# Optimization experiments

Measured on AMD Instinct MI355X. Metric: run time of the kernel, lower is better.

Reference implementation:

```python
import jax, jax.numpy as jnp
import numpy as np

NODE = 100000
REL = 2000
E = 600000  # n_edges == triple_size
D = 128
DEPTH = 2
HEADS = 1


def setup_inputs() -> dict:
    key = jax.random.key(0)
    ks = jax.random.split(key, 8)
    features = jax.random.normal(ks[0], (NODE, D), jnp.float32)
    rel_emb = jax.random.normal(ks[1], (REL, D), jnp.float32)
    sp_val = jax.random.uniform(ks[2], (E,), jnp.float32)
    attn_kernels = jax.random.normal(ks[3], (DEPTH, HEADS, 3 * D), jnp.float32) * 0.1
    adj_src = jnp.sort(jax.random.randint(ks[4], (E,), 0, NODE))  # tf.segment_sum needs sorted ids
    adj_dst = jax.random.randint(ks[5], (E,), 0, NODE)
    sp_rel = jax.random.randint(ks[6], (E,), 0, REL)
    sp_row = jnp.arange(E)  # sparse (triple, rel) matrix row indices
    return dict(features=features, rel_emb=rel_emb, sp_val=sp_val,
                attn_kernels=attn_kernels, adj_src=adj_src, adj_dst=adj_dst,
                sp_rel=sp_rel, sp_row=sp_row)


def _segment_softmax(logits, seg, num):
    m = jax.ops.segment_max(logits, seg, num_segments=num)
    e = jnp.exp(logits - m[seg])
    s = jax.ops.segment_sum(e, seg, num_segments=num)
    return e / s[seg]


def reference(features, rel_emb, sp_val, attn_kernels, adj_src, adj_dst, sp_rel, sp_row):
    act = jax.nn.relu
    feats = act(features)
    outputs = [feats]
    for l in range(DEPTH):
        heads = []
        for h in range(HEADS):
            ak = attn_kernels[l, h]  # [3D]
            # sparse (triple x rel) @ rel_emb -> per-edge relation embedding [E, D]
            rels = jax.ops.segment_sum(sp_val[:, None] * rel_emb[sp_rel], sp_row,
                                       num_segments=E)
            # tf.nn.l2_normalize with eps 1e-12
            rels = rels * jax.lax.rsqrt(jnp.maximum(jnp.sum(rels * rels, axis=1,
                                                            keepdims=True), 1e-12))
            neighs = feats[adj_dst]  # [E, D]
            selfs = feats[adj_src]   # [E, D]
            # Householder-style reflection of neighbor features across rels
            proj = jnp.sum(neighs * rels, axis=1, keepdims=True) * rels
            neighs = neighs - 2.0 * proj
            # attention logits: concat([selfs, neighs, rels]) @ ak
            att = selfs @ ak[:D] + neighs @ ak[D:2 * D] + rels @ ak[2 * D:]
            a = _segment_softmax(att, adj_src, NODE)  # tf.sparse_softmax per row
            heads.append(jax.ops.segment_sum(neighs * a[:, None], adj_src,
                                             num_segments=NODE))
        feats = heads[0] if HEADS == 1 else jnp.concatenate(heads, axis=1)
        feats = act(feats)
        outputs.append(feats)
    return jnp.concatenate(outputs, axis=1)  # [NODE, D*(DEPTH+1)]
```

## Files before the change

### kernel.cpp

```cpp
#include <hip/hip_runtime.h>
#include <math.h>
#include <stdint.h>

#define NNODE 100000
#define NREL 2000
#define NEDGE 600000
#define DIM 128
#define OUTC 384

#define RELU_BLOCKS 12500
#define PRE_BLOCKS 500
#define ROW_BLOCKS ((NNODE + 1 + 255) / 256)

typedef float f32x2 __attribute__((ext_vector_type(2)));

__device__ __forceinline__ float wave_sum(float v) {
#pragma unroll
    for (int off = 32; off > 0; off >>= 1)
        v += __shfl_xor(v, off, 64);
    return v;
}

__device__ __forceinline__ unsigned short f2bf(float f) {
    unsigned b = __float_as_uint(f);
    return (unsigned short)((b + 0x7fffu + ((b >> 16) & 1u)) >> 16);
}
__device__ __forceinline__ unsigned pack2(float f0, float f1) {
    return (unsigned)f2bf(f0) | ((unsigned)f2bf(f1) << 16);
}
__device__ __forceinline__ f32x2 bf2(unsigned u) {
    f32x2 r;
    r.x = __uint_as_float(u << 16);
    r.y = __uint_as_float(u & 0xffff0000u);
    return r;
}

__global__ void k_setup(const float* __restrict__ f, const float* __restrict__ rel,
                        const float* __restrict__ attn, const int* __restrict__ adj_src,
                        float* __restrict__ out, unsigned short* __restrict__ fm,
                        unsigned short* __restrict__ relm,
                        float* __restrict__ relnorm2, float* __restrict__ rdB,
                        float* __restrict__ rdC,
                        float* __restrict__ selfdot0, float* __restrict__ neighdot0,
                        int* __restrict__ row_ptr) {
    int b = blockIdx.x;
    if (b < RELU_BLOCKS) {
        int idx = b * 256 + threadIdx.x;
        int n = idx >> 5;
        int q = idx & 31;
        float4 v = reinterpret_cast<const float4*>(f + (size_t)n * DIM)[q];
        v.x = fmaxf(v.x, 0.f); v.y = fmaxf(v.y, 0.f);
        v.z = fmaxf(v.z, 0.f); v.w = fmaxf(v.w, 0.f);
        reinterpret_cast<float4*>(out + (size_t)n * OUTC)[q] = v;
        uint2 p;
        p.x = pack2(v.x, v.y);
        p.y = pack2(v.z, v.w);
        reinterpret_cast<uint2*>(fm + (size_t)n * DIM)[q] = p;
        float4 a = reinterpret_cast<const float4*>(attn)[q];
        float4 bb = reinterpret_cast<const float4*>(attn + DIM)[q];
        float pa = v.x * a.x + v.y * a.y + v.z * a.z + v.w * a.w;
        float pb = v.x * bb.x + v.y * bb.y + v.z * bb.z + v.w * bb.w;
#pragma unroll
        for (int off = 1; off <= 16; off <<= 1) {
            pa += __shfl_xor(pa, off, 64);
            pb += __shfl_xor(pb, off, 64);
        }
        if (q == 0) { selfdot0[n] = pa; neighdot0[n] = pb; }
    } else if (b < RELU_BLOCKS + PRE_BLOCKS) {
        int wid = (b - RELU_BLOCKS) * 4 + (threadIdx.x >> 6);
        int lane = threadIdx.x & 63;
        float2 v = reinterpret_cast<const float2*>(rel + (size_t)wid * DIM)[lane];
        reinterpret_cast<unsigned*>(relm + (size_t)wid * DIM)[lane] = pack2(v.x, v.y);
        float2 b0 = reinterpret_cast<const float2*>(attn + DIM)[lane];
        float2 c0 = reinterpret_cast<const float2*>(attn + 2 * DIM)[lane];
        float2 b1 = reinterpret_cast<const float2*>(attn + 3 * DIM + DIM)[lane];
        float2 c1 = reinterpret_cast<const float2*>(attn + 3 * DIM + 2 * DIM)[lane];
        float n2  = wave_sum(v.x * v.x + v.y * v.y);
        float pb0 = wave_sum(v.x * b0.x + v.y * b0.y);
        float pc0 = wave_sum(v.x * c0.x + v.y * c0.y);
        float pb1 = wave_sum(v.x * b1.x + v.y * b1.y);
        float pc1 = wave_sum(v.x * c1.x + v.y * c1.y);
        if (lane == 0) {
            relnorm2[wid] = n2;
            rdB[wid] = pb0;        rdC[wid] = pc0;
            rdB[NREL + wid] = pb1; rdC[NREL + wid] = pc1;
        }
    } else {
        int n = (b - RELU_BLOCKS - PRE_BLOCKS) * 256 + threadIdx.x;
        if (n <= NNODE) {
            int lo = 0, hi = NEDGE;
            while (lo < hi) {
                int mid = (lo + hi) >> 1;
                if (adj_src[mid] < n) lo = mid + 1; else hi = mid;
            }
            row_ptr[n] = lo;
        }
    }
}

__global__ void k_edges(const float* __restrict__ sp_val, const int* __restrict__ sp_rel,
                        const int* __restrict__ adj_dst,
                        const float* __restrict__ relnorm2,
                        const float* __restrict__ rdB, const float* __restrict__ rdC,
                        float4* __restrict__ ed0, float4* __restrict__ ed1) {
    int e = blockIdx.x * blockDim.x + threadIdx.x;
    if (e >= NEDGE) return;
    float v = sp_val[e];
    int r = sp_rel[e];
    float n2 = relnorm2[r];
    float sc = v * rsqrtf(fmaxf(v * v * n2, 1e-12f));
    float q2 = 2.f * sc * sc;
    unsigned pk = ((unsigned)adj_dst[e] << 11) | (unsigned)r;
    float pkf = __uint_as_float(pk);
    ed0[e] = make_float4(sc * rdC[r],        q2 * rdB[r],        q2, pkf);
    ed1[e] = make_float4(sc * rdC[NREL + r], q2 * rdB[NREL + r], q2, pkf);
}

template<int USE_ED, int WRITE_NEXT>
__global__ void k_gat(const unsigned short* __restrict__ fin_m,
                      float* __restrict__ fout,
                      unsigned short* __restrict__ fout_m,
                      const unsigned short* __restrict__ relm,
                      const float4* __restrict__ edata,
                      const int* __restrict__ adj_dst, const int* __restrict__ sp_rel,
                      const float* __restrict__ sp_val, const float* __restrict__ relnorm2,
                      const float* __restrict__ rdB, const float* __restrict__ rdC,
                      const float* __restrict__ selfdot, const float* __restrict__ neighdot,
                      const int* __restrict__ row_ptr,
                      float* __restrict__ sd_n, float* __restrict__ nd_n,
                      const float* __restrict__ ak_next) {
    int wv = (blockIdx.x * blockDim.x + threadIdx.x) >> 6;
    int lane = threadIdx.x & 63;
    int g = lane >> 4, gl = lane & 15;
    int node = wv * 4 + g;
    if (node >= NNODE) return;
    int e0 = row_ptr[node], e1 = row_ptr[node + 1];
    float sd = selfdot[node];

    f32x2 acc0 = 0.f, acc1 = 0.f, acc2 = 0.f, acc3 = 0.f;
    float m = -3.0e38f, s = 0.f;

    uint4 fb = make_uint4(0, 0, 0, 0), rb = make_uint4(0, 0, 0, 0);
    float ab = 0.f, qb = 0.f, q2 = 0.f;
    int e = e0;
    if (e < e1) {
        int dst, r;
        if (USE_ED) {
            float4 ed = edata[e];
            unsigned pk = __float_as_uint(ed.w);
            dst = (int)(pk >> 11); r = (int)(pk & 2047u);
            ab = sd + ed.x + neighdot[dst];
            qb = ed.y; q2 = ed.z;
        } else {
            dst = adj_dst[e]; r = sp_rel[e];
            float v = sp_val[e];
            float sc = v * rsqrtf(fmaxf(v * v * relnorm2[r], 1e-12f));
            q2 = 2.f * sc * sc;
            qb = q2 * rdB[r];
            ab = sd + sc * rdC[r] + neighdot[dst];
        }
        fb = *reinterpret_cast<const uint4*>(fin_m + (size_t)dst * DIM + gl * 8);
        rb = *reinterpret_cast<const uint4*>(relm + (size_t)r * DIM + gl * 8);
    }
    while (e < e1) {
        int en = e + 1;
        bool more = en < e1;
        uint4 fb2 = make_uint4(0, 0, 0, 0), rb2 = make_uint4(0, 0, 0, 0);
        float ab2 = 0.f, qb2 = 0.f, q22 = 0.f;
        if (more) {
            int dst, r;
            if (USE_ED) {
                float4 ed = edata[en];
                unsigned pk = __float_as_uint(ed.w);
                dst = (int)(pk >> 11); r = (int)(pk & 2047u);
                ab2 = sd + ed.x + neighdot[dst];
                qb2 = ed.y; q22 = ed.z;
            } else {
                dst = adj_dst[en]; r = sp_rel[en];
                float v = sp_val[en];
                float sc = v * rsqrtf(fmaxf(v * v * relnorm2[r], 1e-12f));
                q22 = 2.f * sc * sc;
                qb2 = q22 * rdB[r];
                ab2 = sd + sc * rdC[r] + neighdot[dst];
            }
            fb2 = *reinterpret_cast<const uint4*>(fin_m + (size_t)dst * DIM + gl * 8);
            rb2 = *reinterpret_cast<const uint4*>(relm + (size_t)r * DIM + gl * 8);
        }
        f32x2 f0 = bf2(fb.x), f1 = bf2(fb.y), f2 = bf2(fb.z), f3 = bf2(fb.w);
        f32x2 r0 = bf2(rb.x), r1 = bf2(rb.y), r2 = bf2(rb.z), r3 = bf2(rb.w);
        f32x2 d2 = f0 * r0;
        d2 += f1 * r1;
        d2 += f2 * r2;
        d2 += f3 * r3;
        float dot = d2.x + d2.y;
        dot += __shfl_xor(dot, 1, 64);
        dot += __shfl_xor(dot, 2, 64);
        dot += __shfl_xor(dot, 4, 64);
        dot += __shfl_xor(dot, 8, 64);
        float att = ab - dot * qb;
        float k2 = dot * q2;
        float nm = fmaxf(m, att);
        float corr = __expf(m - nm);
        float w = __expf(att - nm);
        s = s * corr + w;
        acc0 = acc0 * corr + w * (f0 - k2 * r0);
        acc1 = acc1 * corr + w * (f1 - k2 * r1);
        acc2 = acc2 * corr + w * (f2 - k2 * r2);
        acc3 = acc3 * corr + w * (f3 - k2 * r3);
        m = nm;
        e = en;
        fb = fb2; rb = rb2; ab = ab2; qb = qb2; q2 = q22;
    }

    float inv = (s > 0.f) ? 1.f / s : 0.f;
    float o[8];
    o[0] = fmaxf(acc0.x * inv, 0.f); o[1] = fmaxf(acc0.y * inv, 0.f);
    o[2] = fmaxf(acc1.x * inv, 0.f); o[3] = fmaxf(acc1.y * inv, 0.f);
    o[4] = fmaxf(acc2.x * inv, 0.f); o[5] = fmaxf(acc2.y * inv, 0.f);
    o[6] = fmaxf(acc3.x * inv, 0.f); o[7] = fmaxf(acc3.y * inv, 0.f);
    float4* op = reinterpret_cast<float4*>(fout + (size_t)node * OUTC + gl * 8);
    op[0] = make_float4(o[0], o[1], o[2], o[3]);
    op[1] = make_float4(o[4], o[5], o[6], o[7]);
    if (WRITE_NEXT) {
        uint4 mw;
        mw.x = pack2(o[0], o[1]); mw.y = pack2(o[2], o[3]);
        mw.z = pack2(o[4], o[5]); mw.w = pack2(o[6], o[7]);
        *reinterpret_cast<uint4*>(fout_m + (size_t)node * DIM + gl * 8) = mw;
        const float4* aA = reinterpret_cast<const float4*>(ak_next) + gl * 2;
        const float4* aB = reinterpret_cast<const float4*>(ak_next + DIM) + gl * 2;
        float4 a0 = aA[0], a1 = aA[1], b0 = aB[0], b1 = aB[1];
        float pa = o[0] * a0.x + o[1] * a0.y + o[2] * a0.z + o[3] * a0.w
                 + o[4] * a1.x + o[5] * a1.y + o[6] * a1.z + o[7] * a1.w;
        float pb = o[0] * b0.x + o[1] * b0.y + o[2] * b0.z + o[3] * b0.w
                 + o[4] * b1.x + o[5] * b1.y + o[6] * b1.z + o[7] * b1.w;
#pragma unroll
        for (int off = 1; off <= 8; off <<= 1) {
            pa += __shfl_xor(pa, off, 64);
            pb += __shfl_xor(pb, off, 64);
        }
        if (gl == 0) { sd_n[node] = pa; nd_n[node] = pb; }
    }
}

extern "C" void kernel_launch(void* const* d_in, const int* in_sizes, int n_in,
                              void* d_out, int out_size, void* d_ws, size_t ws_size,
                              hipStream_t stream) {
    const float* features = (const float*)d_in[0];
    const float* rel_emb  = (const float*)d_in[1];
    const float* sp_val   = (const float*)d_in[2];
    const float* attn     = (const float*)d_in[3];
    const int*   adj_src  = (const int*)d_in[4];
    const int*   adj_dst  = (const int*)d_in[5];
    const int*   sp_rel   = (const int*)d_in[6];
    float* out = (float*)d_out;

    char* p = (char*)d_ws;
    unsigned short* mir0 = (unsigned short*)p; p += (size_t)NNODE * DIM * 2;
    unsigned short* mir1 = (unsigned short*)p; p += (size_t)NNODE * DIM * 2;
    unsigned short* relm = (unsigned short*)p; p += (size_t)NREL * DIM * 2;
    float* sd0      = (float*)p; p += (size_t)NNODE * 4;
    float* nd0      = (float*)p; p += (size_t)NNODE * 4;
    float* sd1      = (float*)p; p += (size_t)NNODE * 4;
    float* nd1      = (float*)p; p += (size_t)NNODE * 4;
    float* relnorm2 = (float*)p; p += (size_t)NREL * 4;
    float* rdB      = (float*)p; p += (size_t)2 * NREL * 4;
    float* rdC      = (float*)p; p += (size_t)2 * NREL * 4;
    int*   row_ptr  = (int*)p;   p += (size_t)(NNODE + 1) * 4;
    p = (char*)(((uintptr_t)p + 15) & ~(uintptr_t)15);
    float4* ed0 = (float4*)p; p += (size_t)NEDGE * 16;
    float4* ed1 = (float4*)p; p += (size_t)NEDGE * 16;
    size_t needed = (size_t)(p - (char*)d_ws);
    bool use_ed = (ws_size >= needed);

    k_setup<<<RELU_BLOCKS + PRE_BLOCKS + ROW_BLOCKS, 256, 0, stream>>>(
        features, rel_emb, attn, adj_src, out, mir0, relm,
        relnorm2, rdB, rdC, sd0, nd0, row_ptr);

    int gat_blocks = (NNODE / 4 * 64) / 256;

    if (use_ed) {
        k_edges<<<(NEDGE + 255) / 256, 256, 0, stream>>>(
            sp_val, sp_rel, adj_dst, relnorm2, rdB, rdC, ed0, ed1);
        k_gat<1, 1><<<gat_blocks, 256, 0, stream>>>(
            mir0, out + DIM, mir1, relm, ed0, adj_dst, sp_rel, sp_val, relnorm2,
            rdB, rdC, sd0, nd0, row_ptr, sd1, nd1, attn + 3 * DIM);
        k_gat<1, 0><<<gat_blocks, 256, 0, stream>>>(
            mir1, out + 2 * DIM, (unsigned short*)nullptr, relm, ed1, adj_dst, sp_rel,
            sp_val, relnorm2, rdB + NREL, rdC + NREL, sd1, nd1, row_ptr,
            (float*)nullptr, (float*)nullptr, (const float*)nullptr);
    } else {
        k_gat<0, 1><<<gat_blocks, 256, 0, stream>>>(
            mir0, out + DIM, mir1, relm, (const float4*)nullptr, adj_dst, sp_rel,
            sp_val, relnorm2, rdB, rdC, sd0, nd0, row_ptr, sd1, nd1, attn + 3 * DIM);
        k_gat<0, 0><<<gat_blocks, 256, 0, stream>>>(
            mir1, out + 2 * DIM, (unsigned short*)nullptr, relm, (const float4*)nullptr,
            adj_dst, sp_rel, sp_val, relnorm2, rdB + NREL, rdC + NREL, sd1, nd1, row_ptr,
            (float*)nullptr, (float*)nullptr, (const float*)nullptr);
    }
}
```

Measured before the change: 144.3 us.

## Drop self-term and running max from segment softmax, fold neighbor dot into edge data

The self-attention term is constant within each source-node segment, so it cancels in the softmax and is removed, along with the selfdot arrays. The online-softmax running max and rescaling are dropped, and exp2 is used with log2e pre-folded into the edge coefficients. The layer-0 neighbor dot is folded into the precomputed edge record, removing a gather per edge. Without max subtraction, large logits could overflow exp, and 32-bit index arithmetic replaces size_t.

After: 144.8 us. Within noise of the previous version (+0.3%).

```diff
diff --git a/kernel.cpp b/kernel.cpp
--- a/kernel.cpp
+++ b/kernel.cpp
@@ -7,6 +7,7 @@
 #define NEDGE 600000
 #define DIM 128
 #define OUTC 384
+#define LOG2E 1.4426950408889634f
 
 #define RELU_BLOCKS 12500
 #define PRE_BLOCKS 500
@@ -41,8 +42,7 @@
                         unsigned short* __restrict__ relm,
                         float* __restrict__ relnorm2, float* __restrict__ rdB,
                         float* __restrict__ rdC,
-                        float* __restrict__ selfdot0, float* __restrict__ neighdot0,
-                        int* __restrict__ row_ptr) {
+                        float* __restrict__ nd0, int* __restrict__ row_ptr) {
     int b = blockIdx.x;
     if (b < RELU_BLOCKS) {
         int idx = b * 256 + threadIdx.x;
@@ -56,16 +56,12 @@
         p.x = pack2(v.x, v.y);
         p.y = pack2(v.z, v.w);
         reinterpret_cast<uint2*>(fm + (size_t)n * DIM)[q] = p;
-        float4 a = reinterpret_cast<const float4*>(attn)[q];
         float4 bb = reinterpret_cast<const float4*>(attn + DIM)[q];
-        float pa = v.x * a.x + v.y * a.y + v.z * a.z + v.w * a.w;
         float pb = v.x * bb.x + v.y * bb.y + v.z * bb.z + v.w * bb.w;
 #pragma unroll
-        for (int off = 1; off <= 16; off <<= 1) {
-            pa += __shfl_xor(pa, off, 64);
+        for (int off = 1; off <= 16; off <<= 1)
             pb += __shfl_xor(pb, off, 64);
-        }
-        if (q == 0) { selfdot0[n] = pa; neighdot0[n] = pb; }
+        if (q == 0) nd0[n] = pb * LOG2E;
     } else if (b < RELU_BLOCKS + PRE_BLOCKS) {
         int wid = (b - RELU_BLOCKS) * 4 + (threadIdx.x >> 6);
         int lane = threadIdx.x & 63;
@@ -102,21 +98,24 @@
                         const int* __restrict__ adj_dst,
                         const float* __restrict__ relnorm2,
                         const float* __restrict__ rdB, const float* __restrict__ rdC,
+                        const float* __restrict__ nd0,
                         float4* __restrict__ ed0, float4* __restrict__ ed1) {
     int e = blockIdx.x * blockDim.x + threadIdx.x;
     if (e >= NEDGE) return;
     float v = sp_val[e];
     int r = sp_rel[e];
+    int dst = adj_dst[e];
     float n2 = relnorm2[r];
     float sc = v * rsqrtf(fmaxf(v * v * n2, 1e-12f));
     float q2 = 2.f * sc * sc;
-    unsigned pk = ((unsigned)adj_dst[e] << 11) | (unsigned)r;
+    float scl = sc * LOG2E, q2l = q2 * LOG2E;
+    unsigned pk = ((unsigned)dst << 11) | (unsigned)r;
     float pkf = __uint_as_float(pk);
-    ed0[e] = make_float4(sc * rdC[r],        q2 * rdB[r],        q2, pkf);
-    ed1[e] = make_float4(sc * rdC[NREL + r], q2 * rdB[NREL + r], q2, pkf);
-}
-
-template<int USE_ED, int WRITE_NEXT>
+    ed0[e] = make_float4(nd0[dst] + scl * rdC[r], q2l * rdB[r], q2, pkf);
+    ed1[e] = make_float4(scl * rdC[NREL + r], q2l * rdB[NREL + r], q2, pkf);
+}
+
+template<int USE_ED, int NDFOLD, int WRITE_NEXT>
 __global__ void k_gat(const unsigned short* __restrict__ fin_m,
                       float* __restrict__ fout,
                       unsigned short* __restrict__ fout_m,
@@ -125,20 +124,19 @@
                       const int* __restrict__ adj_dst, const int* __restrict__ sp_rel,
                       const float* __restrict__ sp_val, const float* __restrict__ relnorm2,
                       const float* __restrict__ rdB, const float* __restrict__ rdC,
-                      const float* __restrict__ selfdot, const float* __restrict__ neighdot,
+                      const float* __restrict__ ndpre,
                       const int* __restrict__ row_ptr,
-                      float* __restrict__ sd_n, float* __restrict__ nd_n,
-                      const float* __restrict__ ak_next) {
+                      float* __restrict__ nd_n,
+                      const float* __restrict__ akB_next) {
     int wv = (blockIdx.x * blockDim.x + threadIdx.x) >> 6;
     int lane = threadIdx.x & 63;
     int g = lane >> 4, gl = lane & 15;
     int node = wv * 4 + g;
     if (node >= NNODE) return;
     int e0 = row_ptr[node], e1 = row_ptr[node + 1];
-    float sd = selfdot[node];
 
     f32x2 acc0 = 0.f, acc1 = 0.f, acc2 = 0.f, acc3 = 0.f;
-    float m = -3.0e38f, s = 0.f;
+    float s = 0.f;
 
     uint4 fb = make_uint4(0, 0, 0, 0), rb = make_uint4(0, 0, 0, 0);
     float ab = 0.f, qb = 0.f, q2 = 0.f;
@@ -149,42 +147,41 @@
             float4 ed = edata[e];
             unsigned pk = __float_as_uint(ed.w);
             dst = (int)(pk >> 11); r = (int)(pk & 2047u);
-            ab = sd + ed.x + neighdot[dst];
+            ab = NDFOLD ? ed.x : ed.x + ndpre[dst];
             qb = ed.y; q2 = ed.z;
         } else {
             dst = adj_dst[e]; r = sp_rel[e];
             float v = sp_val[e];
             float sc = v * rsqrtf(fmaxf(v * v * relnorm2[r], 1e-12f));
             q2 = 2.f * sc * sc;
-            qb = q2 * rdB[r];
-            ab = sd + sc * rdC[r] + neighdot[dst];
-        }
-        fb = *reinterpret_cast<const uint4*>(fin_m + (size_t)dst * DIM + gl * 8);
-        rb = *reinterpret_cast<const uint4*>(relm + (size_t)r * DIM + gl * 8);
+            qb = q2 * LOG2E * rdB[r];
+            ab = ndpre[dst] + sc * LOG2E * rdC[r];
+        }
+        fb = *reinterpret_cast<const uint4*>(fin_m + (unsigned)((dst << 7) + (gl << 3)));
+        rb = *reinterpret_cast<const uint4*>(relm + (unsigned)((r << 7) + (gl << 3)));
     }
     while (e < e1) {
         int en = e + 1;
-        bool more = en < e1;
         uint4 fb2 = make_uint4(0, 0, 0, 0), rb2 = make_uint4(0, 0, 0, 0);
         float ab2 = 0.f, qb2 = 0.f, q22 = 0.f;
-        if (more) {
+        if (en < e1) {
             int dst, r;
             if (USE_ED) {
                 float4 ed = edata[en];
                 unsigned pk = __float_as_uint(ed.w);
                 dst = (int)(pk >> 11); r = (int)(pk & 2047u);
-                ab2 = sd + ed.x + neighdot[dst];
+                ab2 = NDFOLD ? ed.x : ed.x + ndpre[dst];
                 qb2 = ed.y; q22 = ed.z;
             } else {
                 dst = adj_dst[en]; r = sp_rel[en];
                 float v = sp_val[en];
                 float sc = v * rsqrtf(fmaxf(v * v * relnorm2[r], 1e-12f));
                 q22 = 2.f * sc * sc;
-                qb2 = q22 * rdB[r];
-                ab2 = sd + sc * rdC[r] + neighdot[dst];
+                qb2 = q22 * LOG2E * rdB[r];
+                ab2 = ndpre[dst] + sc * LOG2E * rdC[r];
             }
-            fb2 = *reinterpret_cast<const uint4*>(fin_m + (size_t)dst * DIM + gl * 8);
-            rb2 = *reinterpret_cast<const uint4*>(relm + (size_t)r * DIM + gl * 8);
+            fb2 = *reinterpret_cast<const uint4*>(fin_m + (unsigned)((dst << 7) + (gl << 3)));
+            rb2 = *reinterpret_cast<const uint4*>(relm + (unsigned)((r << 7) + (gl << 3)));
         }
         f32x2 f0 = bf2(fb.x), f1 = bf2(fb.y), f2 = bf2(fb.z), f3 = bf2(fb.w);
         f32x2 r0 = bf2(rb.x), r1 = bf2(rb.y), r2 = bf2(rb.z), r3 = bf2(rb.w);
@@ -197,17 +194,13 @@
         dot += __shfl_xor(dot, 2, 64);
         dot += __shfl_xor(dot, 4, 64);
         dot += __shfl_xor(dot, 8, 64);
-        float att = ab - dot * qb;
+        float w = __builtin_exp2f(ab - dot * qb);
         float k2 = dot * q2;
-        float nm = fmaxf(m, att);
-        float corr = __expf(m - nm);
-        float w = __expf(att - nm);
-        s = s * corr + w;
-        acc0 = acc0 * corr + w * (f0 - k2 * r0);
-        acc1 = acc1 * corr + w * (f1 - k2 * r1);
-        acc2 = acc2 * corr + w * (f2 - k2 * r2);
-        acc3 = acc3 * corr + w * (f3 - k2 * r3);
-        m = nm;
+        s += w;
+        acc0 += w * (f0 - k2 * r0);
+        acc1 += w * (f1 - k2 * r1);
+        acc2 += w * (f2 - k2 * r2);
+        acc3 += w * (f3 - k2 * r3);
         e = en;
         fb = fb2; rb = rb2; ab = ab2; qb = qb2; q2 = q22;
     }
@@ -218,27 +211,22 @@
     o[2] = fmaxf(acc1.x * inv, 0.f); o[3] = fmaxf(acc1.y * inv, 0.f);
     o[4] = fmaxf(acc2.x * inv, 0.f); o[5] = fmaxf(acc2.y * inv, 0.f);
     o[6] = fmaxf(acc3.x * inv, 0.f); o[7] = fmaxf(acc3.y * inv, 0.f);
-    float4* op = reinterpret_cast<float4*>(fout + (size_t)node * OUTC + gl * 8);
+    float4* op = reinterpret_cast<float4*>(fout + (unsigned)(node * OUTC + gl * 8));
     op[0] = make_float4(o[0], o[1], o[2], o[3]);
     op[1] = make_float4(o[4], o[5], o[6], o[7]);
     if (WRITE_NEXT) {
         uint4 mw;
         mw.x = pack2(o[0], o[1]); mw.y = pack2(o[2], o[3]);
         mw.z = pack2(o[4], o[5]); mw.w = pack2(o[6], o[7]);
-        *reinterpret_cast<uint4*>(fout_m + (size_t)node * DIM + gl * 8) = mw;
-        const float4* aA = reinterpret_cast<const float4*>(ak_next) + gl * 2;
-        const float4* aB = reinterpret_cast<const float4*>(ak_next + DIM) + gl * 2;
-        float4 a0 = aA[0], a1 = aA[1], b0 = aB[0], b1 = aB[1];
-        float pa = o[0] * a0.x + o[1] * a0.y + o[2] * a0.z + o[3] * a0.w
-                 + o[4] * a1.x + o[5] * a1.y + o[6] * a1.z + o[7] * a1.w;
+        *reinterpret_cast<uint4*>(fout_m + (unsigned)((node << 7) + (gl << 3))) = mw;
+        const float4* aB = reinterpret_cast<const float4*>(akB_next) + gl * 2;
+        float4 b0 = aB[0], b1 = aB[1];
         float pb = o[0] * b0.x + o[1] * b0.y + o[2] * b0.z + o[3] * b0.w
                  + o[4] * b1.x + o[5] * b1.y + o[6] * b1.z + o[7] * b1.w;
 #pragma unroll
-        for (int off = 1; off <= 8; off <<= 1) {
-            pa += __shfl_xor(pa, off, 64);
+        for (int off = 1; off <= 8; off <<= 1)
             pb += __shfl_xor(pb, off, 64);
-        }
-        if (gl == 0) { sd_n[node] = pa; nd_n[node] = pb; }
+        if (gl == 0) nd_n[node] = pb * LOG2E;
     }
 }
 
@@ -258,9 +246,7 @@
     unsigned short* mir0 = (unsigned short*)p; p += (size_t)NNODE * DIM * 2;
     unsigned short* mir1 = (unsigned short*)p; p += (size_t)NNODE * DIM * 2;
     unsigned short* relm = (unsigned short*)p; p += (size_t)NREL * DIM * 2;
-    float* sd0      = (float*)p; p += (size_t)NNODE * 4;
     float* nd0      = (float*)p; p += (size_t)NNODE * 4;
-    float* sd1      = (float*)p; p += (size_t)NNODE * 4;
     float* nd1      = (float*)p; p += (size_t)NNODE * 4;
     float* relnorm2 = (float*)p; p += (size_t)NREL * 4;
     float* rdB      = (float*)p; p += (size_t)2 * NREL * 4;
@@ -274,27 +260,28 @@
 
     k_setup<<<RELU_BLOCKS + PRE_BLOCKS + ROW_BLOCKS, 256, 0, stream>>>(
         features, rel_emb, attn, adj_src, out, mir0, relm,
-        relnorm2, rdB, rdC, sd0, nd0, row_ptr);
+        relnorm2, rdB, rdC, nd0, row_ptr);
 
     int gat_blocks = (NNODE / 4 * 64) / 256;
+    const float* akB1 = attn + 3 * DIM + DIM;
 
     if (use_ed) {
         k_edges<<<(NEDGE + 255) / 256, 256, 0, stream>>>(
-            sp_val, sp_rel, adj_dst, relnorm2, rdB, rdC, ed0, ed1);
-        k_gat<1, 1><<<gat_blocks, 256, 0, stream>>>(
+            sp_val, sp_rel, adj_dst, relnorm2, rdB, rdC, nd0, ed0, ed1);
+        k_gat<1, 1, 1><<<gat_blocks, 256, 0, stream>>>(
             mir0, out + DIM, mir1, relm, ed0, adj_dst, sp_rel, sp_val, relnorm2,
-            rdB, rdC, sd0, nd0, row_ptr, sd1, nd1, attn + 3 * DIM);
-        k_gat<1, 0><<<gat_blocks, 256, 0, stream>>>(
+            rdB, rdC, nd0, row_ptr, nd1, akB1);
+        k_gat<1, 0, 0><<<gat_blocks, 256, 0, stream>>>(
             mir1, out + 2 * DIM, (unsigned short*)nullptr, relm, ed1, adj_dst, sp_rel,
-            sp_val, relnorm2, rdB + NREL, rdC + NREL, sd1, nd1, row_ptr,
-            (float*)nullptr, (float*)nullptr, (const float*)nullptr);
+            sp_val, relnorm2, rdB + NREL, rdC + NREL, nd1, row_ptr,
+            (float*)nullptr, (const float*)nullptr);
     } else {
-        k_gat<0, 1><<<gat_blocks, 256, 0, stream>>>(
+        k_gat<0, 0, 1><<<gat_blocks, 256, 0, stream>>>(
             mir0, out + DIM, mir1, relm, (const float4*)nullptr, adj_dst, sp_rel,
-            sp_val, relnorm2, rdB, rdC, sd0, nd0, row_ptr, sd1, nd1, attn + 3 * DIM);
-        k_gat<0, 0><<<gat_blocks, 256, 0, stream>>>(
+            sp_val, relnorm2, rdB, rdC, nd0, row_ptr, nd1, akB1);
+        k_gat<0, 0, 0><<<gat_blocks, 256, 0, stream>>>(
             mir1, out + 2 * DIM, (unsigned short*)nullptr, relm, (const float4*)nullptr,
-            adj_dst, sp_rel, sp_val, relnorm2, rdB + NREL, rdC + NREL, sd1, nd1, row_ptr,
-            (float*)nullptr, (float*)nullptr, (const float*)nullptr);
-    }
-}
+            adj_dst, sp_rel, sp_val, relnorm2, rdB + NREL, rdC + NREL, nd1, row_ptr,
+            (float*)nullptr, (const float*)nullptr);
+    }
+}
```
